# Kernel optimization log

Measured on AMD Instinct MI355X. Metric: run time of the kernel, lower is better.

## Reference

```python
import jax, jax.numpy as jnp
import numpy as np

B, H, DK, DV = 64, 32, 128, 128


def setup_inputs() -> dict:
    key = jax.random.key(0)
    ks = jax.random.split(key, 6)
    return {
        "S": jax.random.normal(ks[0], (B, H, DK, DV), dtype=jnp.float32),
        "k": jax.random.normal(ks[1], (B, H, DK), dtype=jnp.float32),
        "v": jax.random.normal(ks[2], (B, H, DV), dtype=jnp.float32),
        "q": jax.random.normal(ks[3], (B, H, DK), dtype=jnp.float32),
        "alpha": jax.random.uniform(ks[4], (B, H, DK), dtype=jnp.float32),
        "beta": jax.random.uniform(ks[5], (B, H, 1), dtype=jnp.float32),
    }


def reference(S, k, v, q, alpha, beta):
    # S_t = (I - beta k k^T) Diag(alpha) S_{t-1} + beta k v^T ;  o_t = S_t^T q
    S_decay = alpha[..., None] * S                              # (B,H,dk,dv)
    kT_S = jnp.einsum('bhd,bhdv->bhv', k, S_decay)              # k^T (Diag(a) S)
    kkT_S = k[..., :, None] * kT_S[..., None, :]                # outer(k, k^T S)
    kvT = k[..., :, None] * v[..., None, :]                     # outer(k, v)
    S_new = S_decay - beta[..., None] * kkT_S + beta[..., None] * kvT
    o = jnp.einsum('bhdv,bhd->bhv', S_new, q)
    return (S_new, o)
```

## Files before the change

kernel.cpp:

```cpp
#include <hip/hip_runtime.h>


#define DK 128
#define DV 128

typedef float v4f __attribute__((ext_vector_type(4)));
typedef float v2f __attribute__((ext_vector_type(2)));

__global__ __launch_bounds__(256) void kda_update_kernel(
    const float* __restrict__ S,
    const float* __restrict__ k,
    const float* __restrict__ v,
    const float* __restrict__ q,
    const float* __restrict__ alpha,
    const float* __restrict__ beta,
    float* __restrict__ Sout,
    float* __restrict__ o)
{
    const int bh   = blockIdx.x;
    const int tid  = threadIdx.x;
    const int col4 = (tid & 31) * 4;
    const int rgrp = tid >> 5;
    const int d0   = rgrp * 16;

    __shared__ float sa[DK];
    __shared__ float sk[DK];
    __shared__ float sak[DK];
    __shared__ float sqa[DK];
    __shared__ float scoef[DV];
    __shared__ v2f   red[8][DV];
    __shared__ float sqk[2];

    const size_t hoff = (size_t)bh * DK * DV;
    const float* __restrict__ Sbh = S + hoff;

    if (tid < DK) {
        const float kk = k[(size_t)bh * DK + tid];
        const float aa = alpha[(size_t)bh * DK + tid];
        const float qq = q[(size_t)bh * DK + tid];
        sk[tid]  = kk;
        sa[tid]  = aa;
        sak[tid] = kk * aa;
        sqa[tid] = qq * aa;
        float p = qq * kk;
        p += __shfl_xor(p, 32);
        p += __shfl_xor(p, 16);
        p += __shfl_xor(p, 8);
        p += __shfl_xor(p, 4);
        p += __shfl_xor(p, 2);
        p += __shfl_xor(p, 1);
        if ((tid & 63) == 0) sqk[tid >> 6] = p;
    }
    __syncthreads();

    float s_reg[16][4];
    v4f kts = {0.f, 0.f, 0.f, 0.f};
    v4f qas = {0.f, 0.f, 0.f, 0.f};

    #pragma unroll
    for (int i = 0; i < 16; ++i) {
        const int d = d0 + i;
        const v4f sv = *reinterpret_cast<const v4f*>(Sbh + (size_t)d * DV + col4);
        s_reg[i][0] = sv.x; s_reg[i][1] = sv.y; s_reg[i][2] = sv.z; s_reg[i][3] = sv.w;
        kts += sak[d] * sv;
        qas += sqa[d] * sv;
    }

    red[rgrp][col4 + 0] = (v2f){kts.x, qas.x};
    red[rgrp][col4 + 1] = (v2f){kts.y, qas.y};
    red[rgrp][col4 + 2] = (v2f){kts.z, qas.z};
    red[rgrp][col4 + 3] = (v2f){kts.w, qas.w};
    __syncthreads();

    if (tid < DV) {
        v2f acc = {0.f, 0.f};
        #pragma unroll
        for (int g = 0; g < 8; ++g) acc += red[g][tid];
        const float coef = beta[bh] * (v[(size_t)bh * DV + tid] - acc.x);
        scoef[tid] = coef;
        const float qk = sqk[0] + sqk[1];
        o[(size_t)bh * DV + tid] = acc.y + qk * coef;
    }
    __syncthreads();

    const float c0 = scoef[col4 + 0];
    const float c1 = scoef[col4 + 1];
    const float c2 = scoef[col4 + 2];
    const float c3 = scoef[col4 + 3];

    float* __restrict__ Sobh = Sout + hoff;
    #pragma unroll
    for (int i = 0; i < 16; ++i) {
        const int d = d0 + i;
        const float a  = sa[d];
        const float kk = sk[d];
        v4f ov;
        ov.x = a * s_reg[i][0] + kk * c0;
        ov.y = a * s_reg[i][1] + kk * c1;
        ov.z = a * s_reg[i][2] + kk * c2;
        ov.w = a * s_reg[i][3] + kk * c3;
        __builtin_nontemporal_store(ov, reinterpret_cast<v4f*>(Sobh + (size_t)d * DV + col4));
    }
}

extern "C" void kernel_launch(void* const* d_in, const int* in_sizes, int n_in,
                              void* d_out, int out_size, void* d_ws, size_t ws_size,
                              hipStream_t stream) {
    const float* S     = (const float*)d_in[0];
    const float* k     = (const float*)d_in[1];
    const float* v     = (const float*)d_in[2];
    const float* q     = (const float*)d_in[3];
    const float* alpha = (const float*)d_in[4];
    const float* beta  = (const float*)d_in[5];

    const int BH = in_sizes[5];

    float* Sout = (float*)d_out;
    float* o    = Sout + (size_t)BH * DK * DV;

    kda_update_kernel<<<dim3(BH), dim3(256), 0, stream>>>(S, k, v, q, alpha, beta, Sout, o);
}
```

Before: 47.04 us.

## Process two heads per block, overlapping second head's loads with first head's stores

Each block now handles two (b,h) heads. The S tile for the second head is loaded and reduced while the first head's output tile is being written, so global loads and stores overlap within a block. The grid is halved to 1024 blocks, and the first phase uses all 256 threads to stage the per-head vectors. In exchange, register pressure roughly doubles (two 64-float tiles are held at once), which may lower occupancy. The code also assumes BH is even.

```diff
diff --git a/kernel.cpp b/kernel.cpp
--- a/kernel.cpp
+++ b/kernel.cpp
@@ -5,7 +5,6 @@
 #define DV 128
 
 typedef float v4f __attribute__((ext_vector_type(4)));
-typedef float v2f __attribute__((ext_vector_type(2)));
 
 __global__ __launch_bounds__(256) void kda_update_kernel(
     const float* __restrict__ S,
@@ -17,31 +16,33 @@
     float* __restrict__ Sout,
     float* __restrict__ o)
 {
-    const int bh   = blockIdx.x;
     const int tid  = threadIdx.x;
     const int col4 = (tid & 31) * 4;
     const int rgrp = tid >> 5;
     const int d0   = rgrp * 16;
 
-    __shared__ float sa[DK];
-    __shared__ float sk[DK];
-    __shared__ float sak[DK];
-    __shared__ float sqa[DK];
+    __shared__ float sa[2][DK];
+    __shared__ float sk[2][DK];
+    __shared__ float sak[2][DK];
+    __shared__ float sqa[2][DK];
     __shared__ float scoef[DV];
-    __shared__ v2f   red[8][DV];
-    __shared__ float sqk[2];
+    __shared__ float redk[8][DV];
+    __shared__ float redq[8][DV];
+    __shared__ float sqk[2][2];
 
-    const size_t hoff = (size_t)bh * DK * DV;
-    const float* __restrict__ Sbh = S + hoff;
+    const int bh0 = blockIdx.x * 2;
 
-    if (tid < DK) {
-        const float kk = k[(size_t)bh * DK + tid];
-        const float aa = alpha[(size_t)bh * DK + tid];
-        const float qq = q[(size_t)bh * DK + tid];
-        sk[tid]  = kk;
-        sa[tid]  = aa;
-        sak[tid] = kk * aa;
-        sqa[tid] = qq * aa;
+    {
+        const int t  = tid >> 7;
+        const int i  = tid & 127;
+        const int bh = bh0 + t;
+        const float kk = k[(size_t)bh * DK + i];
+        const float aa = alpha[(size_t)bh * DK + i];
+        const float qq = q[(size_t)bh * DK + i];
+        sk[t][i]  = kk;
+        sa[t][i]  = aa;
+        sak[t][i] = kk * aa;
+        sqa[t][i] = qq * aa;
         float p = qq * kk;
         p += __shfl_xor(p, 32);
         p += __shfl_xor(p, 16);
@@ -49,57 +50,110 @@
         p += __shfl_xor(p, 4);
         p += __shfl_xor(p, 2);
         p += __shfl_xor(p, 1);
-        if ((tid & 63) == 0) sqk[tid >> 6] = p;
+        if ((tid & 63) == 0) sqk[t][i >> 6] = p;
     }
     __syncthreads();
 
-    float s_reg[16][4];
-    v4f kts = {0.f, 0.f, 0.f, 0.f};
-    v4f qas = {0.f, 0.f, 0.f, 0.f};
+    const size_t hoff0 = (size_t)bh0 * DK * DV;
+    const size_t hoff1 = hoff0 + (size_t)DK * DV;
+    const float* __restrict__ Sb0 = S + hoff0;
+    const float* __restrict__ Sb1 = S + hoff1;
 
+    float sA[16][4];
+    v4f ktsA = {0.f, 0.f, 0.f, 0.f};
+    v4f qasA = {0.f, 0.f, 0.f, 0.f};
     #pragma unroll
     for (int i = 0; i < 16; ++i) {
         const int d = d0 + i;
-        const v4f sv = *reinterpret_cast<const v4f*>(Sbh + (size_t)d * DV + col4);
-        s_reg[i][0] = sv.x; s_reg[i][1] = sv.y; s_reg[i][2] = sv.z; s_reg[i][3] = sv.w;
-        kts += sak[d] * sv;
-        qas += sqa[d] * sv;
+        const v4f sv = *reinterpret_cast<const v4f*>(Sb0 + (size_t)d * DV + col4);
+        sA[i][0] = sv.x; sA[i][1] = sv.y; sA[i][2] = sv.z; sA[i][3] = sv.w;
+        ktsA += sak[0][d] * sv;
+        qasA += sqa[0][d] * sv;
     }
-
-    red[rgrp][col4 + 0] = (v2f){kts.x, qas.x};
-    red[rgrp][col4 + 1] = (v2f){kts.y, qas.y};
-    red[rgrp][col4 + 2] = (v2f){kts.z, qas.z};
-    red[rgrp][col4 + 3] = (v2f){kts.w, qas.w};
+    redk[rgrp][col4 + 0] = ktsA.x; redk[rgrp][col4 + 1] = ktsA.y;
+    redk[rgrp][col4 + 2] = ktsA.z; redk[rgrp][col4 + 3] = ktsA.w;
+    redq[rgrp][col4 + 0] = qasA.x; redq[rgrp][col4 + 1] = qasA.y;
+    redq[rgrp][col4 + 2] = qasA.z; redq[rgrp][col4 + 3] = qasA.w;
     __syncthreads();
 
     if (tid < DV) {
-        v2f acc = {0.f, 0.f};
+        float a1 = 0.f, a2 = 0.f;
         #pragma unroll
-        for (int g = 0; g < 8; ++g) acc += red[g][tid];
-        const float coef = beta[bh] * (v[(size_t)bh * DV + tid] - acc.x);
+        for (int g = 0; g < 8; ++g) { a1 += redk[g][tid]; a2 += redq[g][tid]; }
+        const float coef = beta[bh0] * (v[(size_t)bh0 * DV + tid] - a1);
         scoef[tid] = coef;
-        const float qk = sqk[0] + sqk[1];
-        o[(size_t)bh * DV + tid] = acc.y + qk * coef;
+        o[(size_t)bh0 * DV + tid] = a2 + (sqk[0][0] + sqk[0][1]) * coef;
     }
     __syncthreads();
 
-    const float c0 = scoef[col4 + 0];
-    const float c1 = scoef[col4 + 1];
-    const float c2 = scoef[col4 + 2];
-    const float c3 = scoef[col4 + 3];
+    float c0 = scoef[col4 + 0];
+    float c1 = scoef[col4 + 1];
+    float c2 = scoef[col4 + 2];
+    float c3 = scoef[col4 + 3];
 
-    float* __restrict__ Sobh = Sout + hoff;
+    float sB[16][4];
+    v4f ktsB = {0.f, 0.f, 0.f, 0.f};
+    v4f qasB = {0.f, 0.f, 0.f, 0.f};
     #pragma unroll
     for (int i = 0; i < 16; ++i) {
         const int d = d0 + i;
-        const float a  = sa[d];
-        const float kk = sk[d];
-        v4f ov;
-        ov.x = a * s_reg[i][0] + kk * c0;
-        ov.y = a * s_reg[i][1] + kk * c1;
-        ov.z = a * s_reg[i][2] + kk * c2;
-        ov.w = a * s_reg[i][3] + kk * c3;
-        __builtin_nontemporal_store(ov, reinterpret_cast<v4f*>(Sobh + (size_t)d * DV + col4));
+        const v4f sv = *reinterpret_cast<const v4f*>(Sb1 + (size_t)d * DV + col4);
+        sB[i][0] = sv.x; sB[i][1] = sv.y; sB[i][2] = sv.z; sB[i][3] = sv.w;
+        ktsB += sak[1][d] * sv;
+        qasB += sqa[1][d] * sv;
+    }
+
+    {
+        float* __restrict__ So0 = Sout + hoff0;
+        #pragma unroll
+        for (int i = 0; i < 16; ++i) {
+            const int d = d0 + i;
+            const float a  = sa[0][d];
+            const float kk = sk[0][d];
+            v4f ov;
+            ov.x = a * sA[i][0] + kk * c0;
+            ov.y = a * sA[i][1] + kk * c1;
+            ov.z = a * sA[i][2] + kk * c2;
+            ov.w = a * sA[i][3] + kk * c3;
+            __builtin_nontemporal_store(ov, reinterpret_cast<v4f*>(So0 + (size_t)d * DV + col4));
+        }
+    }
+
+    redk[rgrp][col4 + 0] = ktsB.x; redk[rgrp][col4 + 1] = ktsB.y;
+    redk[rgrp][col4 + 2] = ktsB.z; redk[rgrp][col4 + 3] = ktsB.w;
+    redq[rgrp][col4 + 0] = qasB.x; redq[rgrp][col4 + 1] = qasB.y;
+    redq[rgrp][col4 + 2] = qasB.z; redq[rgrp][col4 + 3] = qasB.w;
+    __syncthreads();
+
+    if (tid < DV) {
+        float a1 = 0.f, a2 = 0.f;
+        #pragma unroll
+        for (int g = 0; g < 8; ++g) { a1 += redk[g][tid]; a2 += redq[g][tid]; }
+        const float coef = beta[bh0 + 1] * (v[(size_t)(bh0 + 1) * DV + tid] - a1);
+        scoef[tid] = coef;
+        o[(size_t)(bh0 + 1) * DV + tid] = a2 + (sqk[1][0] + sqk[1][1]) * coef;
+    }
+    __syncthreads();
+
+    c0 = scoef[col4 + 0];
+    c1 = scoef[col4 + 1];
+    c2 = scoef[col4 + 2];
+    c3 = scoef[col4 + 3];
+
+    {
+        float* __restrict__ So1 = Sout + hoff1;
+        #pragma unroll
+        for (int i = 0; i < 16; ++i) {
+            const int d = d0 + i;
+            const float a  = sa[1][d];
+            const float kk = sk[1][d];
+            v4f ov;
+            ov.x = a * sB[i][0] + kk * c0;
+            ov.y = a * sB[i][1] + kk * c1;
+            ov.z = a * sB[i][2] + kk * c2;
+            ov.w = a * sB[i][3] + kk * c3;
+            __builtin_nontemporal_store(ov, reinterpret_cast<v4f*>(So1 + (size_t)d * DV + col4));
+        }
     }
 }
 
@@ -118,5 +172,5 @@
     float* Sout = (float*)d_out;
     float* o    = Sout + (size_t)BH * DK * DV;
 
-    kda_update_kernel<<<dim3(BH), dim3(256), 0, stream>>>(S, k, v, q, alpha, beta, Sout, o);
+    kda_update_kernel<<<dim3(BH / 2), dim3(256), 0, stream>>>(S, k, v, q, alpha, beta, Sout, o);
 }
```

Result: no change. 47.39 us (+0.7%).
